# Kernel optimization log

Hardware: AMD Instinct MI355X
Metric: run time of the kernel (lower is better)

Reference implementation:

```python
import jax, jax.numpy as jnp
import numpy as np

TOP_K = 2

def setup_inputs() -> dict:
    key = jax.random.key(0)
    k0, k1, k2, k3 = jax.random.split(key, 4)
    B, S, H, I, E = 2, 2048, 1024, 1408, 8
    hidden_states = jax.random.normal(k0, (B, S, H), dtype=jnp.float32)
    router_weight = jax.random.normal(k1, (E, H), dtype=jnp.float32) * 0.02
    gate_up_proj = jax.random.normal(k2, (E, 2 * I, H), dtype=jnp.float32) * 0.02
    down_proj = jax.random.normal(k3, (E, H, I), dtype=jnp.float32) * 0.02
    return {
        "hidden_states": hidden_states,
        "router_weight": router_weight,
        "gate_up_proj": gate_up_proj,
        "down_proj": down_proj,
    }

def reference(hidden_states, router_weight, gate_up_proj, down_proj):
    B, S, H = hidden_states.shape
    E = router_weight.shape[0]
    x = hidden_states.reshape(-1, H)                       # [T, H]
    T = x.shape[0]
    # Router: logits -> float32 softmax -> top-k (matches torch: topk on probs)
    logits = x @ router_weight.T                           # [T, E]
    probs = jax.nn.softmax(logits.astype(jnp.float32), axis=-1)
    topw, topi = jax.lax.top_k(probs, TOP_K)               # [T, K]
    topw = topw.astype(x.dtype)
    # Per-token combine weights over experts (zero for non-selected experts).
    combine = jnp.zeros((T, E), dtype=x.dtype)
    combine = combine.at[jnp.arange(T)[:, None], topi].set(topw)  # [T, E]
    # Dense grouped expert compute (same math as gather-GEMM-scatter loop:
    # tokens not routed to expert e get combine weight 0).
    gu = jnp.einsum('th,eoh->teo', x, gate_up_proj)        # [T, E, 2I]
    g, u = jnp.split(gu, 2, axis=-1)                       # [T, E, I] each
    h = jax.nn.silu(g) * u                                 # [T, E, I]
    y = jnp.einsum('tei,ehi->teh', h, down_proj)           # [T, E, H]
    out = jnp.einsum('teh,te->th', y, combine)             # [T, H]
    return out.reshape(B, S, H)
```

## Files before the change

### kernel.cpp

```cpp
#include <hip/hip_runtime.h>
#include <math.h>

#define NTOK 4096
#define HDIM 1024
#define NEXP 8
#define IDIM 1408
#define TWO_I 2816
#define TM 256
#define TK 64
#define NRB 40
#define ROWCAP (NRB * 256)

#define RT_BLKS 1024
#define CVG_BLKS 2048
#define G1_BLKS 440
#define CVD_BLKS 256

typedef _Float16 f16x8 __attribute__((ext_vector_type(8)));
typedef float f32x4 __attribute__((ext_vector_type(4)));

typedef __attribute__((address_space(1))) const unsigned int gu32;
typedef __attribute__((address_space(3))) unsigned int lu32;
__device__ __forceinline__ void async16(const void* g, void* l) {
  __builtin_amdgcn_global_load_lds((gu32*)g, (lu32*)l, 16, 0, 0);
}

__device__ __forceinline__ void seg_prefix(const int* __restrict__ counts, int* aof) {
  int o = 0; aof[0] = 0;
#pragma unroll
  for (int i = 0; i < 8; i++) { o += (counts[i] + 255) & ~255; aof[i + 1] = o; }
}

__device__ __forceinline__ void cvt8(const float4* __restrict__ s, uint4* __restrict__ d, size_t idx) {
  float4 a = s[idx * 2], b = s[idx * 2 + 1];
  union { _Float16 h[8]; uint4 u; } p;
  p.h[0] = (_Float16)a.x; p.h[1] = (_Float16)a.y; p.h[2] = (_Float16)a.z; p.h[3] = (_Float16)a.w;
  p.h[4] = (_Float16)b.x; p.h[5] = (_Float16)b.y; p.h[6] = (_Float16)b.z; p.h[7] = (_Float16)b.w;
  d[idx] = p.u;
}

#define NG8 (NEXP * TWO_I * HDIM / 8)
#define ND8 (NEXP * HDIM * IDIM / 8)

extern "C" __global__ void moe_rcv(const float* __restrict__ x,
                                   const float* __restrict__ rw,
                                   int* __restrict__ topi,
                                   float* __restrict__ topw,
                                   _Float16* __restrict__ xh,
                                   const float* __restrict__ gup,
                                   _Float16* __restrict__ guph) {
  if (blockIdx.x >= RT_BLKS) {
    size_t idx = (size_t)(blockIdx.x - RT_BLKS) * 256 + threadIdx.x;
    const float4* s = (const float4*)gup; uint4* d = (uint4*)guph;
    for (; idx < NG8; idx += (size_t)CVG_BLKS * 256) cvt8(s, d, idx);
    return;
  }
  int w = threadIdx.x >> 6, lane = threadIdx.x & 63;
  int t = blockIdx.x * 4 + w;
  const float4* xp = (const float4*)(x + (size_t)t * HDIM);
  const float4* rp = (const float4*)rw;
  float acc[NEXP];
#pragma unroll
  for (int e = 0; e < NEXP; e++) acc[e] = 0.f;
#pragma unroll
  for (int i = 0; i < HDIM / 256; i++) {
    float4 xv = xp[i * 64 + lane];
    union { _Float16 h[4]; uint2 u; } pk;
    pk.h[0] = (_Float16)xv.x; pk.h[1] = (_Float16)xv.y;
    pk.h[2] = (_Float16)xv.z; pk.h[3] = (_Float16)xv.w;
    *(uint2*)(xh + (size_t)t * HDIM + i * 256 + lane * 4) = pk.u;
#pragma unroll
    for (int e = 0; e < NEXP; e++) {
      float4 rv = rp[e * 256 + i * 64 + lane];
      acc[e] += xv.x * rv.x + xv.y * rv.y + xv.z * rv.z + xv.w * rv.w;
    }
  }
#pragma unroll
  for (int e = 0; e < NEXP; e++) {
#pragma unroll
    for (int off = 32; off > 0; off >>= 1) acc[e] += __shfl_down(acc[e], off);
  }
  if (lane == 0) {
    float m = acc[0];
    for (int e = 1; e < NEXP; e++) m = fmaxf(m, acc[e]);
    float p[NEXP], s = 0.f;
    for (int e = 0; e < NEXP; e++) { p[e] = __expf(acc[e] - m); s += p[e]; }
    float inv = 1.f / s;
    int i0 = 0; float b0 = p[0];
    for (int e = 1; e < NEXP; e++) if (p[e] > b0) { b0 = p[e]; i0 = e; }
    int i1 = -1; float b1 = -1.f;
    for (int e = 0; e < NEXP; e++) if (e != i0 && p[e] > b1) { b1 = p[e]; i1 = e; }
    topi[t * 2] = i0; topi[t * 2 + 1] = i1;
    topw[t * 2] = b0 * inv; topw[t * 2 + 1] = b1 * inv;
  }
}

extern "C" __global__ void moe_count(const int* __restrict__ topi, int* __restrict__ cnt_part) {
  __shared__ int cnt[NEXP];
  if (threadIdx.x < NEXP) cnt[threadIdx.x] = 0;
  __syncthreads();
  int t = blockIdx.x * 256 + threadIdx.x;
  atomicAdd(&cnt[topi[t * 2]], 1);
  atomicAdd(&cnt[topi[t * 2 + 1]], 1);
  __syncthreads();
  if (threadIdx.x < NEXP) cnt_part[blockIdx.x * NEXP + threadIdx.x] = cnt[threadIdx.x];
}

extern "C" __global__ void moe_scatter(const int* __restrict__ topi, const float* __restrict__ topw,
                                       const int* __restrict__ cnt_part, int* __restrict__ counts,
                                       int* __restrict__ tok, float* __restrict__ wrow,
                                       int* __restrict__ rows) {
  __shared__ int part_l[16 * NEXP];
  __shared__ int cnt[NEXP];
  __shared__ int base[NEXP];
  __shared__ int tot_l[NEXP];
  const int tid = threadIdx.x, blk = blockIdx.x;
  if (tid < 16 * NEXP) part_l[tid] = cnt_part[tid];
  if (tid < NEXP) cnt[tid] = 0;
  __syncthreads();
  if (tid < NEXP) {
    int tot = 0, pre = 0;
#pragma unroll
    for (int b = 0; b < 16; b++) {
      int v = part_l[b * NEXP + tid];
      tot += v;
      if (b < blk) pre += v;
    }
    tot_l[tid] = tot;
    base[tid] = pre;
  }
  __syncthreads();
  if (tid < NEXP) {
    int o = 0;
    for (int i = 0; i < tid; i++) o += (tot_l[i] + 255) & ~255;
    base[tid] += o;
    if (blk == 0) counts[tid] = tot_l[tid];
  }
  __syncthreads();
  int t = blk * 256 + tid;
  int e0 = topi[t * 2], e1 = topi[t * 2 + 1];
  int r0 = atomicAdd(&cnt[e0], 1);
  int r1 = atomicAdd(&cnt[e1], 1);
  int row0 = base[e0] + r0;
  int row1 = base[e1] + r1;
  tok[row0] = t; wrow[row0] = topw[t * 2];     rows[t * 2]     = row0;
  tok[row1] = t; wrow[row1] = topw[t * 2 + 1]; rows[t * 2 + 1] = row1;
}

#define WAITVM(n) asm volatile("s_waitcnt vmcnt(" #n ")" ::: "memory")
#define BAR() __builtin_amdgcn_s_barrier()
#define PRIO(x) __builtin_amdgcn_s_setprio(x)

#define LDV(off) (*(const f16x8*)((const char*)smem + (uint32_t)(off)))

#define RD_A(grp, BO) { \
  _Pragma("unroll") for (int m_ = 0; m_ < 4; m_++) { \
    va[m_][0] = LDV(sA0 + (BO) + ((grp)*4 + m_)*2048); \
    va[m_][1] = LDV(sA1 + (BO) + ((grp)*4 + m_)*2048); } }

#define RD_B(VB, nb, BO) { \
  _Pragma("unroll") for (int n_ = 0; n_ < 2; n_++) { \
    VB[n_][0] = LDV(sB0 + (BO) + ((nb)*2 + n_)*2048); \
    VB[n_][1] = LDV(sB1 + (BO) + ((nb)*2 + n_)*2048); } }

#define MM(qa, qb, VB) { \
  _Pragma("unroll") for (int k_ = 0; k_ < 2; k_++) \
  _Pragma("unroll") for (int m_ = 0; m_ < 4; m_++) \
  _Pragma("unroll") for (int n_ = 0; n_ < 2; n_++) \
    acc[(qa)*4 + m_][(qb)*2 + n_] = __builtin_amdgcn_mfma_f32_16x16x32_f16( \
        va[m_][k_], VB[n_][k_], acc[(qa)*4 + m_][(qb)*2 + n_], 0, 0, 0); }

#define STG4(P, bf, r0, kt) { \
  async16(P[0][0] + (kt)*TK, smem + ((bf)*4 + (r0))*8192 + wv*512); \
  async16(P[0][1] + (kt)*TK, smem + ((bf)*4 + (r0))*8192 + 4096 + wv*512); \
  async16(P[1][0] + (kt)*TK, smem + ((bf)*4 + (r0) + 1)*8192 + wv*512); \
  async16(P[1][1] + (kt)*TK, smem + ((bf)*4 + (r0) + 1)*8192 + 4096 + wv*512); }
#define STAGE_A(bf, kt) STG4(pA, bf, 0, kt)
#define STAGE_B(bf, kt) STG4(pB, bf, 2, kt)

#define GEMM_CORE(NIT) { \
  STAGE_B(0, 0); STAGE_A(0, 0); \
  STAGE_B(1, 1); STAGE_A(1, 1); \
  WAITVM(8); BAR(); \
  _Pragma("unroll 1") \
  for (int it = 0; it < (NIT); ++it) { \
    const int nl = (it + 1 < (NIT)); \
    const int kt2 = 2*it + 2, kt3 = 2*it + 3; \
     RD_B(vb0, 0, 0); RD_A(0, 0); BAR(); PRIO(1); MM(0,0,vb0); PRIO(0); BAR(); \
     RD_B(vb1, 1, 0); BAR(); PRIO(1); MM(0,1,vb1); PRIO(0); BAR(); \
     RD_A(1, 0); if (nl) STAGE_B(0, kt2); BAR(); PRIO(1); MM(1,0,vb0); PRIO(0); BAR(); \
     if (nl) { STAGE_A(0, kt2); } PRIO(1); MM(1,1,vb1); PRIO(0); \
              if (nl) { WAITVM(8); } else { WAITVM(0); } BAR(); \
     RD_B(vb0, 0, 65536); RD_A(0, 65536); BAR(); PRIO(1); MM(0,0,vb0); PRIO(0); BAR(); \
     RD_B(vb1, 1, 65536); BAR(); PRIO(1); MM(0,1,vb1); PRIO(0); BAR(); \
     RD_A(1, 65536); if (nl) STAGE_B(1, kt3); BAR(); PRIO(1); MM(1,0,vb0); PRIO(0); BAR(); \
     if (nl) { STAGE_A(1, kt3); } PRIO(1); MM(1,1,vb1); PRIO(0); \
              if (nl) { WAITVM(8); } BAR(); \
  } \
  asm volatile("" ::: "memory"); }

#define GEMM_SETUP() \
  const int lane = tid & 63, wv = tid >> 6; \
  const int wm = wv >> 2, wn = wv & 3; \
  const int quad = lane >> 4, l15 = lane & 15; \
  const int srow = tid >> 3; \
  const int kc = ((tid & 7) ^ (srow & 7)) << 3; \
  const uint32_t c0 = (uint32_t)((quad * 16) ^ ((l15 & 7) << 4)); \
  const uint32_t c1 = c0 ^ 64; \
  const uint32_t sA0 = wm * 16384 + l15 * 128 + c0; \
  const uint32_t sA1 = wm * 16384 + l15 * 128 + c1; \
  const uint32_t sB0 = (2 + (wn >> 1)) * 16384 + ((wn & 1) * 64 + l15) * 128 + c0; \
  const uint32_t sB1 = (2 + (wn >> 1)) * 16384 + ((wn & 1) * 64 + l15) * 128 + c1; \
  f32x4 acc[8][4]; \
  _Pragma("unroll") for (int m = 0; m < 8; m++) \
  _Pragma("unroll") for (int n = 0; n < 4; n++) acc[m][n] = (f32x4){0.f, 0.f, 0.f, 0.f}; \
  f16x8 va[4][2], vb0[2][2], vb1[2][2];

extern "C" __global__ __launch_bounds__(512, 2) void moe_gemm1cd(
    const _Float16* __restrict__ xh, const _Float16* __restrict__ guph,
    const int* __restrict__ counts, const int* __restrict__ tok,
    _Float16* __restrict__ hbuf,
    const float* __restrict__ dp, _Float16* __restrict__ dph) {
  __shared__ __align__(128) _Float16 smem[65536];
  const int tid = threadIdx.x;
  const int fid = blockIdx.x;
  if (fid >= G1_BLKS) {
    size_t idx = (size_t)(fid - G1_BLKS) * 512 + tid;
    const float4* s = (const float4*)dp; uint4* d = (uint4*)dph;
    for (; idx < ND8; idx += (size_t)CVD_BLKS * 512) cvt8(s, d, idx);
    return;
  }
  int aof[9]; seg_prefix(counts, aof);
  const int g = fid & 7, t7 = fid >> 3;
  const int j = t7 / 5, r5 = t7 - j * 5;
  const int rb = g + 8 * r5;
  const int row0 = rb * TM;
  if (row0 >= aof[8]) return;
  int e = 0;
#pragma unroll
  for (int i = 0; i < 8; i++) if (row0 >= aof[i]) e = i;
  const int lim = aof[e] + counts[e];

  GEMM_SETUP();

  const _Float16* pA[2][2]; const _Float16* pB[2][2];
#pragma unroll
  for (int h = 0; h < 2; h++)
#pragma unroll
    for (int q = 0; q < 2; q++) {
      int rowi = row0 + h * 128 + q * 64 + srow;
      int tv = tok[rowi];
      int tk = (rowi < lim) ? tv : 0;
      pA[h][q] = xh + (size_t)tk * HDIM + kc;
    }
  const _Float16* eb = guph + (size_t)e * TWO_I * HDIM;
#pragma unroll
  for (int q = 0; q < 2; q++) {
    pB[0][q] = eb + (size_t)(j * 128 + q * 64 + srow) * HDIM + kc;
    pB[1][q] = eb + (size_t)(IDIM + j * 128 + q * 64 + srow) * HDIM + kc;
  }

  GEMM_CORE(HDIM / (2 * TK))

  if (wn >= 2) {
#pragma unroll
    for (int mf = 0; mf < 8; mf++)
#pragma unroll
      for (int nf = 0; nf < 4; nf++)
#pragma unroll
        for (int r2 = 0; r2 < 4; r2++)
          smem[(wm * 128 + mf * 16 + quad * 4 + r2) * 132 + (wn - 2) * 64 + nf * 16 + l15] =
              (_Float16)acc[mf][nf][r2];
  }
  __syncthreads();
  if (wn < 2) {
#pragma unroll
    for (int mf = 0; mf < 8; mf++) {
#pragma unroll
      for (int r2 = 0; r2 < 4; r2++) {
        const int rl = wm * 128 + mf * 16 + quad * 4 + r2;
        _Float16* orow = hbuf + (size_t)(row0 + rl) * IDIM + j * 128 + wn * 64;
#pragma unroll
        for (int nf = 0; nf < 4; nf++) {
          float gg = acc[mf][nf][r2];
          float uu = (float)smem[rl * 132 + wn * 64 + nf * 16 + l15];
          float hh = gg / (1.f + __expf(-gg)) * uu;
          orow[nf * 16 + l15] = (_Float16)hh;
        }
      }
    }
  }
}

extern "C" __global__ __launch_bounds__(256, 2) void moe_gemm2(
    const _Float16* __restrict__ hbuf, const _Float16* __restrict__ dph,
    const int* __restrict__ counts, const float* __restrict__ wrow,
    _Float16* __restrict__ yh) {
  __shared__ __align__(128) _Float16 smem[32768];
  int aof[9]; seg_prefix(counts, aof);
  const int fid = blockIdx.x;
  const int g = fid & 7, t7 = fid >> 3;
  const int cb = t7 / 10, r10 = t7 - cb * 10;
  const int rb = g + 8 * r10;
  const int row0 = rb * 128;
  if (row0 >= aof[8]) return;
  int e = 0;
#pragma unroll
  for (int i = 0; i < 8; i++) if (row0 >= aof[i]) e = i;

  const int tid = threadIdx.x;
  const int lane = tid & 63, wv = tid >> 6;
  const int wm = wv >> 1, wn = wv & 1;
  const int quad = lane >> 4, l15 = lane & 15;
  const int kc = ((tid & 7) ^ ((tid >> 3) & 7)) << 3;
  const uint32_t c0 = (uint32_t)((quad * 16) ^ ((l15 & 7) << 4));
  const uint32_t c1 = c0 ^ 64;
  const uint32_t sA_0 = (uint32_t)((wm * 64 + l15) * 128) + c0;
  const uint32_t sA_1 = (uint32_t)((wm * 64 + l15) * 128) + c1;
  const uint32_t sB_0 = 16384u + (uint32_t)((wn * 64 + l15) * 128) + c0;
  const uint32_t sB_1 = 16384u + (uint32_t)((wn * 64 + l15) * 128) + c1;

  f32x4 acc2[4][4];
#pragma unroll
  for (int m = 0; m < 4; m++)
#pragma unroll
    for (int n = 0; n < 4; n++) acc2[m][n] = (f32x4){0.f, 0.f, 0.f, 0.f};
  f16x8 va2[4][2], vb2[4][2];

  const _Float16* pA2[4]; const _Float16* pB2[4];
  const _Float16* eb = dph + (size_t)e * HDIM * IDIM;
#pragma unroll
  for (int c = 0; c < 4; c++) {
    pA2[c] = hbuf + (size_t)(row0 + c * 32 + (tid >> 3)) * IDIM + kc;
    pB2[c] = eb + (size_t)(cb * 128 + c * 32 + (tid >> 3)) * IDIM + kc;
  }

#define STG2(bf, kt) { \
  _Pragma("unroll") for (int c_ = 0; c_ < 4; c_++) { \
    async16(pA2[c_] + (kt)*TK, smem + (bf)*16384 + c_*2048 + tid*8); \
    async16(pB2[c_] + (kt)*TK, smem + (bf)*16384 + 8192 + c_*2048 + tid*8); } }

  const int NIT2 = IDIM / TK;
  STG2(0, 0); STG2(1, 1);
  WAITVM(8); BAR();
#pragma unroll 1
  for (int kt = 0; kt < NIT2; ++kt) {
    const uint32_t BO = (kt & 1) ? 32768u : 0u;
#pragma unroll
    for (int m_ = 0; m_ < 4; m_++) {
      va2[m_][0] = LDV(sA_0 + BO + m_ * 2048);
      va2[m_][1] = LDV(sA_1 + BO + m_ * 2048);
    }
#pragma unroll
    for (int n_ = 0; n_ < 4; n_++) {
      vb2[n_][0] = LDV(sB_0 + BO + n_ * 2048);
      vb2[n_][1] = LDV(sB_1 + BO + n_ * 2048);
    }
    asm volatile("s_waitcnt lgkmcnt(0)" ::: "memory");
    BAR();
    if (kt + 2 < NIT2) { STG2((kt & 1), kt + 2); }
    PRIO(1);
#pragma unroll
    for (int k_ = 0; k_ < 2; k_++)
#pragma unroll
      for (int m_ = 0; m_ < 4; m_++)
#pragma unroll
        for (int n_ = 0; n_ < 4; n_++)
          acc2[m_][n_] = __builtin_amdgcn_mfma_f32_16x16x32_f16(
              va2[m_][k_], vb2[n_][k_], acc2[m_][n_], 0, 0, 0);
    PRIO(0);
    if (kt + 2 < NIT2) { WAITVM(8); } else { WAITVM(0); }
    BAR();
  }
#undef STG2

#pragma unroll
  for (int mf = 0; mf < 4; mf++) {
#pragma unroll
    for (int r2 = 0; r2 < 4; r2++) {
      const int row = row0 + wm * 64 + mf * 16 + quad * 4 + r2;
      const float wgt = wrow[row];
      _Float16* orow = yh + (size_t)row * HDIM + cb * 128 + wn * 64;
#pragma unroll
      for (int nf = 0; nf < 4; nf++)
        orow[nf * 16 + l15] = (_Float16)(acc2[mf][nf][r2] * wgt);
    }
  }
}

extern "C" __global__ void moe_combine(const _Float16* __restrict__ yh,
                                       const int* __restrict__ rows,
                                       float* __restrict__ out) {
  int i = blockIdx.x * 256 + threadIdx.x;
  int t = i >> 7, c8 = i & 127;
  int rA = rows[t * 2], rB = rows[t * 2 + 1];
  union { uint4 u; _Float16 h[8]; } pa, pb;
  pa.u = ((const uint4*)(yh + (size_t)rA * HDIM))[c8];
  pb.u = ((const uint4*)(yh + (size_t)rB * HDIM))[c8];
  float4 o0, o1;
  o0.x = (float)pa.h[0] + (float)pb.h[0]; o0.y = (float)pa.h[1] + (float)pb.h[1];
  o0.z = (float)pa.h[2] + (float)pb.h[2]; o0.w = (float)pa.h[3] + (float)pb.h[3];
  o1.x = (float)pa.h[4] + (float)pb.h[4]; o1.y = (float)pa.h[5] + (float)pb.h[5];
  o1.z = (float)pa.h[6] + (float)pb.h[6]; o1.w = (float)pa.h[7] + (float)pb.h[7];
  ((float4*)out)[(size_t)i * 2] = o0;
  ((float4*)out)[(size_t)i * 2 + 1] = o1;
}

extern "C" void kernel_launch(void* const* d_in, const int* in_sizes, int n_in,
                              void* d_out, int out_size, void* d_ws, size_t ws_size,
                              hipStream_t stream) {
  const float* x   = (const float*)d_in[0];
  const float* rw  = (const float*)d_in[1];
  const float* gup = (const float*)d_in[2];
  const float* dp  = (const float*)d_in[3];
  float* out = (float*)d_out;

  char* ws = (char*)d_ws;
  int*   counts   = (int*)ws;
  int*   cnt_part = (int*)(ws + 64);
  int*   topi   = (int*)(ws + 4096);
  float* topw   = (float*)(ws + 36864);
  int*   tok    = (int*)(ws + 69632);
  float* wrow   = (float*)(ws + 110592);
  int*   rows   = (int*)(ws + 151552);
  _Float16* xh   = (_Float16*)(ws + 184320);
  _Float16* guph = (_Float16*)(ws + 8572928);
  _Float16* dph  = (_Float16*)(ws + 54710272);
  _Float16* hbuf = (_Float16*)(ws + 77778944);
  _Float16* yh   = (_Float16*)(ws + 8572928);

  moe_rcv<<<RT_BLKS + CVG_BLKS, 256, 0, stream>>>(x, rw, topi, topw, xh, gup, guph);
  moe_count<<<NTOK / 256, 256, 0, stream>>>(topi, cnt_part);
  moe_scatter<<<NTOK / 256, 256, 0, stream>>>(topi, topw, cnt_part, counts, tok, wrow, rows);
  moe_gemm1cd<<<G1_BLKS + CVD_BLKS, 512, 0, stream>>>(xh, guph, counts, tok, hbuf, dp, dph);
  moe_gemm2<<<8 * 8 * 10, 256, 0, stream>>>(hbuf, dph, counts, wrow, yh);
  moe_combine<<<NTOK * HDIM / 8 / 256, 256, 0, stream>>>(yh, rows, out);
}
```

Baseline: 317.1 us.

## Shrink gate-up GEMM tiles to 128x128 and fuse expert counting into router

The first grouped GEMM moves from 256-row tiles with 512-thread blocks and a split-phase schedule to 128-row by 64-column (gate+up) tiles with 256-thread blocks, reusing the simpler double-buffered K-loop shared with the down GEMM. That produces many more blocks (1760 vs 440) and should improve load balance across CUs, but each block reuses less data and runs a simpler pipeline. Expert counting also moves into the router kernel through per-block shared atomics, which removes the separate count launch. The scatter kernel now reduces 1024 partial counts.

```diff
diff --git a/kernel.cpp b/kernel.cpp
--- a/kernel.cpp
+++ b/kernel.cpp
@@ -6,14 +6,13 @@
 #define NEXP 8
 #define IDIM 1408
 #define TWO_I 2816
-#define TM 256
 #define TK 64
-#define NRB 40
-#define ROWCAP (NRB * 256)
+#define ROWCAP 10240
 
 #define RT_BLKS 1024
 #define CVG_BLKS 2048
-#define G1_BLKS 440
+#define G1J 22
+#define G1_BLKS (8 * G1J * 10)
 #define CVD_BLKS 256
 
 typedef _Float16 f16x8 __attribute__((ext_vector_type(8)));
@@ -47,6 +46,7 @@
                                    int* __restrict__ topi,
                                    float* __restrict__ topw,
                                    _Float16* __restrict__ xh,
+                                   int* __restrict__ cnt_part,
                                    const float* __restrict__ gup,
                                    _Float16* __restrict__ guph) {
   if (blockIdx.x >= RT_BLKS) {
@@ -55,6 +55,9 @@
     for (; idx < NG8; idx += (size_t)CVG_BLKS * 256) cvt8(s, d, idx);
     return;
   }
+  __shared__ int c8[NEXP];
+  if (threadIdx.x < NEXP) c8[threadIdx.x] = 0;
+  __syncthreads();
   int w = threadIdx.x >> 6, lane = threadIdx.x & 63;
   int t = blockIdx.x * 4 + w;
   const float4* xp = (const float4*)(x + (size_t)t * HDIM);
@@ -92,37 +95,37 @@
     for (int e = 0; e < NEXP; e++) if (e != i0 && p[e] > b1) { b1 = p[e]; i1 = e; }
     topi[t * 2] = i0; topi[t * 2 + 1] = i1;
     topw[t * 2] = b0 * inv; topw[t * 2 + 1] = b1 * inv;
-  }
-}
-
-extern "C" __global__ void moe_count(const int* __restrict__ topi, int* __restrict__ cnt_part) {
-  __shared__ int cnt[NEXP];
-  if (threadIdx.x < NEXP) cnt[threadIdx.x] = 0;
-  __syncthreads();
-  int t = blockIdx.x * 256 + threadIdx.x;
-  atomicAdd(&cnt[topi[t * 2]], 1);
-  atomicAdd(&cnt[topi[t * 2 + 1]], 1);
-  __syncthreads();
-  if (threadIdx.x < NEXP) cnt_part[blockIdx.x * NEXP + threadIdx.x] = cnt[threadIdx.x];
+    atomicAdd(&c8[i0], 1);
+    atomicAdd(&c8[i1], 1);
+  }
+  __syncthreads();
+  if (threadIdx.x < NEXP) cnt_part[threadIdx.x * 1024 + blockIdx.x] = c8[threadIdx.x];
 }
 
 extern "C" __global__ void moe_scatter(const int* __restrict__ topi, const float* __restrict__ topw,
                                        const int* __restrict__ cnt_part, int* __restrict__ counts,
                                        int* __restrict__ tok, float* __restrict__ wrow,
                                        int* __restrict__ rows) {
-  __shared__ int part_l[16 * NEXP];
+  __shared__ int part16[16 * NEXP];
   __shared__ int cnt[NEXP];
   __shared__ int base[NEXP];
   __shared__ int tot_l[NEXP];
   const int tid = threadIdx.x, blk = blockIdx.x;
-  if (tid < 16 * NEXP) part_l[tid] = cnt_part[tid];
+  if (tid < 128) {
+    int g = tid >> 3, e = tid & 7;
+    const int4* p = (const int4*)(cnt_part + e * 1024 + g * 64);
+    int s = 0;
+#pragma unroll
+    for (int b = 0; b < 16; b++) { int4 v = p[b]; s += v.x + v.y + v.z + v.w; }
+    part16[g * NEXP + e] = s;
+  }
   if (tid < NEXP) cnt[tid] = 0;
   __syncthreads();
   if (tid < NEXP) {
     int tot = 0, pre = 0;
 #pragma unroll
     for (int b = 0; b < 16; b++) {
-      int v = part_l[b * NEXP + tid];
+      int v = part16[b * NEXP + tid];
       tot += v;
       if (b < blk) pre += v;
     }
@@ -150,140 +153,123 @@
 #define WAITVM(n) asm volatile("s_waitcnt vmcnt(" #n ")" ::: "memory")
 #define BAR() __builtin_amdgcn_s_barrier()
 #define PRIO(x) __builtin_amdgcn_s_setprio(x)
-
 #define LDV(off) (*(const f16x8*)((const char*)smem + (uint32_t)(off)))
 
-#define RD_A(grp, BO) { \
-  _Pragma("unroll") for (int m_ = 0; m_ < 4; m_++) { \
-    va[m_][0] = LDV(sA0 + (BO) + ((grp)*4 + m_)*2048); \
-    va[m_][1] = LDV(sA1 + (BO) + ((grp)*4 + m_)*2048); } }
-
-#define RD_B(VB, nb, BO) { \
-  _Pragma("unroll") for (int n_ = 0; n_ < 2; n_++) { \
-    VB[n_][0] = LDV(sB0 + (BO) + ((nb)*2 + n_)*2048); \
-    VB[n_][1] = LDV(sB1 + (BO) + ((nb)*2 + n_)*2048); } }
-
-#define MM(qa, qb, VB) { \
-  _Pragma("unroll") for (int k_ = 0; k_ < 2; k_++) \
-  _Pragma("unroll") for (int m_ = 0; m_ < 4; m_++) \
-  _Pragma("unroll") for (int n_ = 0; n_ < 2; n_++) \
-    acc[(qa)*4 + m_][(qb)*2 + n_] = __builtin_amdgcn_mfma_f32_16x16x32_f16( \
-        va[m_][k_], VB[n_][k_], acc[(qa)*4 + m_][(qb)*2 + n_], 0, 0, 0); }
-
-#define STG4(P, bf, r0, kt) { \
-  async16(P[0][0] + (kt)*TK, smem + ((bf)*4 + (r0))*8192 + wv*512); \
-  async16(P[0][1] + (kt)*TK, smem + ((bf)*4 + (r0))*8192 + 4096 + wv*512); \
-  async16(P[1][0] + (kt)*TK, smem + ((bf)*4 + (r0) + 1)*8192 + wv*512); \
-  async16(P[1][1] + (kt)*TK, smem + ((bf)*4 + (r0) + 1)*8192 + 4096 + wv*512); }
-#define STAGE_A(bf, kt) STG4(pA, bf, 0, kt)
-#define STAGE_B(bf, kt) STG4(pB, bf, 2, kt)
-
-#define GEMM_CORE(NIT) { \
-  STAGE_B(0, 0); STAGE_A(0, 0); \
-  STAGE_B(1, 1); STAGE_A(1, 1); \
+#define STG2(bf, kt) { \
+  _Pragma("unroll") for (int c_ = 0; c_ < 4; c_++) { \
+    async16(pA2[c_] + (size_t)(kt) * TK, smem + (bf) * 16384 + c_ * 2048 + tid * 8); \
+    async16(pB2[c_] + (size_t)(kt) * TK, smem + (bf) * 16384 + 8192 + c_ * 2048 + tid * 8); } }
+
+#define K128_SETUP() \
+  const int lane = tid & 63, wv = tid >> 6; \
+  const int wm = wv >> 1, wn = wv & 1; \
+  const int quad = lane >> 4, l15 = lane & 15; \
+  const int srow8 = tid >> 3; \
+  const int kc = ((tid & 7) ^ (srow8 & 7)) << 3; \
+  const uint32_t c0 = (uint32_t)((quad * 16) ^ ((l15 & 7) << 4)); \
+  const uint32_t c1 = c0 ^ 64; \
+  const uint32_t sA_0 = (uint32_t)((wm * 64 + l15) * 128) + c0; \
+  const uint32_t sA_1 = (uint32_t)((wm * 64 + l15) * 128) + c1; \
+  const uint32_t sB_0 = 16384u + (uint32_t)((wn * 64 + l15) * 128) + c0; \
+  const uint32_t sB_1 = 16384u + (uint32_t)((wn * 64 + l15) * 128) + c1; \
+  f32x4 acc2[4][4]; \
+  _Pragma("unroll") for (int m = 0; m < 4; m++) \
+  _Pragma("unroll") for (int n = 0; n < 4; n++) acc2[m][n] = (f32x4){0.f, 0.f, 0.f, 0.f}; \
+  f16x8 va2[4][2], vb2[4][2];
+
+#define K128_LOOP(NIT) { \
+  STG2(0, 0); STG2(1, 1); \
   WAITVM(8); BAR(); \
   _Pragma("unroll 1") \
-  for (int it = 0; it < (NIT); ++it) { \
-    const int nl = (it + 1 < (NIT)); \
-    const int kt2 = 2*it + 2, kt3 = 2*it + 3; \
-     RD_B(vb0, 0, 0); RD_A(0, 0); BAR(); PRIO(1); MM(0,0,vb0); PRIO(0); BAR(); \
-     RD_B(vb1, 1, 0); BAR(); PRIO(1); MM(0,1,vb1); PRIO(0); BAR(); \
-     RD_A(1, 0); if (nl) STAGE_B(0, kt2); BAR(); PRIO(1); MM(1,0,vb0); PRIO(0); BAR(); \
-     if (nl) { STAGE_A(0, kt2); } PRIO(1); MM(1,1,vb1); PRIO(0); \
-              if (nl) { WAITVM(8); } else { WAITVM(0); } BAR(); \
-     RD_B(vb0, 0, 65536); RD_A(0, 65536); BAR(); PRIO(1); MM(0,0,vb0); PRIO(0); BAR(); \
-     RD_B(vb1, 1, 65536); BAR(); PRIO(1); MM(0,1,vb1); PRIO(0); BAR(); \
-     RD_A(1, 65536); if (nl) STAGE_B(1, kt3); BAR(); PRIO(1); MM(1,0,vb0); PRIO(0); BAR(); \
-     if (nl) { STAGE_A(1, kt3); } PRIO(1); MM(1,1,vb1); PRIO(0); \
-              if (nl) { WAITVM(8); } BAR(); \
-  } \
-  asm volatile("" ::: "memory"); }
-
-#define GEMM_SETUP() \
-  const int lane = tid & 63, wv = tid >> 6; \
-  const int wm = wv >> 2, wn = wv & 3; \
-  const int quad = lane >> 4, l15 = lane & 15; \
-  const int srow = tid >> 3; \
-  const int kc = ((tid & 7) ^ (srow & 7)) << 3; \
-  const uint32_t c0 = (uint32_t)((quad * 16) ^ ((l15 & 7) << 4)); \
-  const uint32_t c1 = c0 ^ 64; \
-  const uint32_t sA0 = wm * 16384 + l15 * 128 + c0; \
-  const uint32_t sA1 = wm * 16384 + l15 * 128 + c1; \
-  const uint32_t sB0 = (2 + (wn >> 1)) * 16384 + ((wn & 1) * 64 + l15) * 128 + c0; \
-  const uint32_t sB1 = (2 + (wn >> 1)) * 16384 + ((wn & 1) * 64 + l15) * 128 + c1; \
-  f32x4 acc[8][4]; \
-  _Pragma("unroll") for (int m = 0; m < 8; m++) \
-  _Pragma("unroll") for (int n = 0; n < 4; n++) acc[m][n] = (f32x4){0.f, 0.f, 0.f, 0.f}; \
-  f16x8 va[4][2], vb0[2][2], vb1[2][2];
-
-extern "C" __global__ __launch_bounds__(512, 2) void moe_gemm1cd(
+  for (int kt = 0; kt < (NIT); ++kt) { \
+    const uint32_t BO = (kt & 1) ? 32768u : 0u; \
+    _Pragma("unroll") for (int m_ = 0; m_ < 4; m_++) { \
+      va2[m_][0] = LDV(sA_0 + BO + m_ * 2048); \
+      va2[m_][1] = LDV(sA_1 + BO + m_ * 2048); } \
+    _Pragma("unroll") for (int n_ = 0; n_ < 4; n_++) { \
+      vb2[n_][0] = LDV(sB_0 + BO + n_ * 2048); \
+      vb2[n_][1] = LDV(sB_1 + BO + n_ * 2048); } \
+    asm volatile("s_waitcnt lgkmcnt(0)" ::: "memory"); \
+    BAR(); \
+    if (kt + 2 < (NIT)) { STG2((kt & 1), kt + 2); } \
+    PRIO(1); \
+    _Pragma("unroll") for (int k_ = 0; k_ < 2; k_++) \
+    _Pragma("unroll") for (int m_ = 0; m_ < 4; m_++) \
+    _Pragma("unroll") for (int n_ = 0; n_ < 4; n_++) \
+      acc2[m_][n_] = __builtin_amdgcn_mfma_f32_16x16x32_f16( \
+          va2[m_][k_], vb2[n_][k_], acc2[m_][n_], 0, 0, 0); \
+    PRIO(0); \
+    if (kt + 2 < (NIT)) { WAITVM(8); } else { WAITVM(0); } \
+    BAR(); \
+  } }
+
+extern "C" __global__ __launch_bounds__(256, 2) void moe_gemm1cd(
     const _Float16* __restrict__ xh, const _Float16* __restrict__ guph,
     const int* __restrict__ counts, const int* __restrict__ tok,
     _Float16* __restrict__ hbuf,
     const float* __restrict__ dp, _Float16* __restrict__ dph) {
-  __shared__ __align__(128) _Float16 smem[65536];
+  __shared__ __align__(128) _Float16 smem[32768];
   const int tid = threadIdx.x;
   const int fid = blockIdx.x;
   if (fid >= G1_BLKS) {
-    size_t idx = (size_t)(fid - G1_BLKS) * 512 + tid;
+    size_t idx = (size_t)(fid - G1_BLKS) * 256 + tid;
     const float4* s = (const float4*)dp; uint4* d = (uint4*)dph;
-    for (; idx < ND8; idx += (size_t)CVD_BLKS * 512) cvt8(s, d, idx);
+    for (; idx < ND8; idx += (size_t)CVD_BLKS * 256) cvt8(s, d, idx);
     return;
   }
   int aof[9]; seg_prefix(counts, aof);
   const int g = fid & 7, t7 = fid >> 3;
-  const int j = t7 / 5, r5 = t7 - j * 5;
-  const int rb = g + 8 * r5;
-  const int row0 = rb * TM;
+  const int j = t7 / 10, r10 = t7 - j * 10;
+  const int rb = g + 8 * r10;
+  const int row0 = rb * 128;
   if (row0 >= aof[8]) return;
   int e = 0;
 #pragma unroll
   for (int i = 0; i < 8; i++) if (row0 >= aof[i]) e = i;
   const int lim = aof[e] + counts[e];
 
-  GEMM_SETUP();
-
-  const _Float16* pA[2][2]; const _Float16* pB[2][2];
-#pragma unroll
-  for (int h = 0; h < 2; h++)
-#pragma unroll
-    for (int q = 0; q < 2; q++) {
-      int rowi = row0 + h * 128 + q * 64 + srow;
-      int tv = tok[rowi];
-      int tk = (rowi < lim) ? tv : 0;
-      pA[h][q] = xh + (size_t)tk * HDIM + kc;
-    }
+  K128_SETUP();
+
+  const _Float16* pA2[4]; const _Float16* pB2[4];
+#pragma unroll
+  for (int c = 0; c < 4; c++) {
+    int rowi = row0 + c * 32 + srow8;
+    int tv = tok[rowi];
+    int tk = (rowi < lim) ? tv : 0;
+    pA2[c] = xh + (size_t)tk * HDIM + kc;
+  }
   const _Float16* eb = guph + (size_t)e * TWO_I * HDIM;
 #pragma unroll
-  for (int q = 0; q < 2; q++) {
-    pB[0][q] = eb + (size_t)(j * 128 + q * 64 + srow) * HDIM + kc;
-    pB[1][q] = eb + (size_t)(IDIM + j * 128 + q * 64 + srow) * HDIM + kc;
-  }
-
-  GEMM_CORE(HDIM / (2 * TK))
-
-  if (wn >= 2) {
-#pragma unroll
-    for (int mf = 0; mf < 8; mf++)
+  for (int c = 0; c < 4; c++) {
+    int brow = (c < 2) ? (j * 64 + c * 32 + srow8)
+                       : (IDIM + j * 64 + (c - 2) * 32 + srow8);
+    pB2[c] = eb + (size_t)brow * HDIM + kc;
+  }
+
+  K128_LOOP(HDIM / TK)
+
+  if (wn == 1) {
+#pragma unroll
+    for (int mf = 0; mf < 4; mf++)
 #pragma unroll
       for (int nf = 0; nf < 4; nf++)
 #pragma unroll
         for (int r2 = 0; r2 < 4; r2++)
-          smem[(wm * 128 + mf * 16 + quad * 4 + r2) * 132 + (wn - 2) * 64 + nf * 16 + l15] =
-              (_Float16)acc[mf][nf][r2];
-  }
-  __syncthreads();
-  if (wn < 2) {
-#pragma unroll
-    for (int mf = 0; mf < 8; mf++) {
+          smem[(wm * 64 + mf * 16 + quad * 4 + r2) * 66 + nf * 16 + l15] =
+              (_Float16)acc2[mf][nf][r2];
+  }
+  __syncthreads();
+  if (wn == 0) {
+#pragma unroll
+    for (int mf = 0; mf < 4; mf++) {
 #pragma unroll
       for (int r2 = 0; r2 < 4; r2++) {
-        const int rl = wm * 128 + mf * 16 + quad * 4 + r2;
-        _Float16* orow = hbuf + (size_t)(row0 + rl) * IDIM + j * 128 + wn * 64;
+        const int rl = wm * 64 + mf * 16 + quad * 4 + r2;
+        _Float16* orow = hbuf + (size_t)(row0 + rl) * IDIM + j * 64;
 #pragma unroll
         for (int nf = 0; nf < 4; nf++) {
-          float gg = acc[mf][nf][r2];
-          float uu = (float)smem[rl * 132 + wn * 64 + nf * 16 + l15];
+          float gg = acc2[mf][nf][r2];
+          float uu = (float)smem[rl * 66 + nf * 16 + l15];
           float hh = gg / (1.f + __expf(-gg)) * uu;
           orow[nf * 16 + l15] = (_Float16)hh;
         }
@@ -309,70 +295,17 @@
   for (int i = 0; i < 8; i++) if (row0 >= aof[i]) e = i;
 
   const int tid = threadIdx.x;
-  const int lane = tid & 63, wv = tid >> 6;
-  const int wm = wv >> 1, wn = wv & 1;
-  const int quad = lane >> 4, l15 = lane & 15;
-  const int kc = ((tid & 7) ^ ((tid >> 3) & 7)) << 3;
-  const uint32_t c0 = (uint32_t)((quad * 16) ^ ((l15 & 7) << 4));
-  const uint32_t c1 = c0 ^ 64;
-  const uint32_t sA_0 = (uint32_t)((wm * 64 + l15) * 128) + c0;
-  const uint32_t sA_1 = (uint32_t)((wm * 64 + l15) * 128) + c1;
-  const uint32_t sB_0 = 16384u + (uint32_t)((wn * 64 + l15) * 128) + c0;
-  const uint32_t sB_1 = 16384u + (uint32_t)((wn * 64 + l15) * 128) + c1;
-
-  f32x4 acc2[4][4];
-#pragma unroll
-  for (int m = 0; m < 4; m++)
-#pragma unroll
-    for (int n = 0; n < 4; n++) acc2[m][n] = (f32x4){0.f, 0.f, 0.f, 0.f};
-  f16x8 va2[4][2], vb2[4][2];
+  K128_SETUP();
 
   const _Float16* pA2[4]; const _Float16* pB2[4];
   const _Float16* eb = dph + (size_t)e * HDIM * IDIM;
 #pragma unroll
   for (int c = 0; c < 4; c++) {
-    pA2[c] = hbuf + (size_t)(row0 + c * 32 + (tid >> 3)) * IDIM + kc;
-    pB2[c] = eb + (size_t)(cb * 128 + c * 32 + (tid >> 3)) * IDIM + kc;
-  }
-
-#define STG2(bf, kt) { \
-  _Pragma("unroll") for (int c_ = 0; c_ < 4; c_++) { \
-    async16(pA2[c_] + (kt)*TK, smem + (bf)*16384 + c_*2048 + tid*8); \
-    async16(pB2[c_] + (kt)*TK, smem + (bf)*16384 + 8192 + c_*2048 + tid*8); } }
-
-  const int NIT2 = IDIM / TK;
-  STG2(0, 0); STG2(1, 1);
-  WAITVM(8); BAR();
-#pragma unroll 1
-  for (int kt = 0; kt < NIT2; ++kt) {
-    const uint32_t BO = (kt & 1) ? 32768u : 0u;
-#pragma unroll
-    for (int m_ = 0; m_ < 4; m_++) {
-      va2[m_][0] = LDV(sA_0 + BO + m_ * 2048);
-      va2[m_][1] = LDV(sA_1 + BO + m_ * 2048);
-    }
-#pragma unroll
-    for (int n_ = 0; n_ < 4; n_++) {
-      vb2[n_][0] = LDV(sB_0 + BO + n_ * 2048);
-      vb2[n_][1] = LDV(sB_1 + BO + n_ * 2048);
-    }
-    asm volatile("s_waitcnt lgkmcnt(0)" ::: "memory");
-    BAR();
-    if (kt + 2 < NIT2) { STG2((kt & 1), kt + 2); }
-    PRIO(1);
-#pragma unroll
-    for (int k_ = 0; k_ < 2; k_++)
-#pragma unroll
-      for (int m_ = 0; m_ < 4; m_++)
-#pragma unroll
-        for (int n_ = 0; n_ < 4; n_++)
-          acc2[m_][n_] = __builtin_amdgcn_mfma_f32_16x16x32_f16(
-              va2[m_][k_], vb2[n_][k_], acc2[m_][n_], 0, 0, 0);
-    PRIO(0);
-    if (kt + 2 < NIT2) { WAITVM(8); } else { WAITVM(0); }
-    BAR();
-  }
-#undef STG2
+    pA2[c] = hbuf + (size_t)(row0 + c * 32 + srow8) * IDIM + kc;
+    pB2[c] = eb + (size_t)(cb * 128 + c * 32 + srow8) * IDIM + kc;
+  }
+
+  K128_LOOP(IDIM / TK)
 
 #pragma unroll
   for (int mf = 0; mf < 4; mf++) {
@@ -418,21 +351,20 @@
   char* ws = (char*)d_ws;
   int*   counts   = (int*)ws;
   int*   cnt_part = (int*)(ws + 64);
-  int*   topi   = (int*)(ws + 4096);
-  float* topw   = (float*)(ws + 36864);
-  int*   tok    = (int*)(ws + 69632);
-  float* wrow   = (float*)(ws + 110592);
-  int*   rows   = (int*)(ws + 151552);
-  _Float16* xh   = (_Float16*)(ws + 184320);
-  _Float16* guph = (_Float16*)(ws + 8572928);
-  _Float16* dph  = (_Float16*)(ws + 54710272);
-  _Float16* hbuf = (_Float16*)(ws + 77778944);
-  _Float16* yh   = (_Float16*)(ws + 8572928);
-
-  moe_rcv<<<RT_BLKS + CVG_BLKS, 256, 0, stream>>>(x, rw, topi, topw, xh, gup, guph);
-  moe_count<<<NTOK / 256, 256, 0, stream>>>(topi, cnt_part);
+  int*   topi   = (int*)(ws + 32832);
+  float* topw   = (float*)(ws + 65600);
+  int*   tok    = (int*)(ws + 98368);
+  float* wrow   = (float*)(ws + 139328);
+  int*   rows   = (int*)(ws + 180288);
+  _Float16* xh   = (_Float16*)(ws + 213056);
+  _Float16* guph = (_Float16*)(ws + 8601664);
+  _Float16* dph  = (_Float16*)(ws + 54739008);
+  _Float16* hbuf = (_Float16*)(ws + 77807680);
+  _Float16* yh   = (_Float16*)(ws + 8601664);
+
+  moe_rcv<<<RT_BLKS + CVG_BLKS, 256, 0, stream>>>(x, rw, topi, topw, xh, cnt_part, gup, guph);
   moe_scatter<<<NTOK / 256, 256, 0, stream>>>(topi, topw, cnt_part, counts, tok, wrow, rows);
-  moe_gemm1cd<<<G1_BLKS + CVD_BLKS, 512, 0, stream>>>(xh, guph, counts, tok, hbuf, dp, dph);
+  moe_gemm1cd<<<G1_BLKS + CVD_BLKS, 256, 0, stream>>>(xh, guph, counts, tok, hbuf, dp, dph);
   moe_gemm2<<<8 * 8 * 10, 256, 0, stream>>>(hbuf, dph, counts, wrow, yh);
   moe_combine<<<NTOK * HDIM / 8 / 256, 256, 0, stream>>>(yh, rows, out);
 }
```

New measurement: 347.6 us. 1.1x slower.

## Fuse expert counting into router, retile down-projection GEMM to 256x256 tiles

Applied to the files above, without the earlier changes.

Expert counting moves into the router kernel: each router block writes per-block counts, and the scatter kernel reduces them, so the separate count launch goes away. The down-projection GEMM changes from 128x128 tiles with 256 threads to the shared 256x256, 512-thread GEMM core used by the first GEMM, which raises data reuse per block but leaves fewer blocks to fill the device. The row-block to block-index mapping also changes from interleaved to contiguous, which may affect L2 locality.

```diff
diff --git a/kernel.cpp b/kernel.cpp
--- a/kernel.cpp
+++ b/kernel.cpp
@@ -47,6 +47,7 @@
                                    int* __restrict__ topi,
                                    float* __restrict__ topw,
                                    _Float16* __restrict__ xh,
+                                   int* __restrict__ cnt_part,
                                    const float* __restrict__ gup,
                                    _Float16* __restrict__ guph) {
   if (blockIdx.x >= RT_BLKS) {
@@ -55,6 +56,9 @@
     for (; idx < NG8; idx += (size_t)CVG_BLKS * 256) cvt8(s, d, idx);
     return;
   }
+  __shared__ int c8[NEXP];
+  if (threadIdx.x < NEXP) c8[threadIdx.x] = 0;
+  __syncthreads();
   int w = threadIdx.x >> 6, lane = threadIdx.x & 63;
   int t = blockIdx.x * 4 + w;
   const float4* xp = (const float4*)(x + (size_t)t * HDIM);
@@ -92,37 +96,37 @@
     for (int e = 0; e < NEXP; e++) if (e != i0 && p[e] > b1) { b1 = p[e]; i1 = e; }
     topi[t * 2] = i0; topi[t * 2 + 1] = i1;
     topw[t * 2] = b0 * inv; topw[t * 2 + 1] = b1 * inv;
-  }
-}
-
-extern "C" __global__ void moe_count(const int* __restrict__ topi, int* __restrict__ cnt_part) {
-  __shared__ int cnt[NEXP];
-  if (threadIdx.x < NEXP) cnt[threadIdx.x] = 0;
-  __syncthreads();
-  int t = blockIdx.x * 256 + threadIdx.x;
-  atomicAdd(&cnt[topi[t * 2]], 1);
-  atomicAdd(&cnt[topi[t * 2 + 1]], 1);
-  __syncthreads();
-  if (threadIdx.x < NEXP) cnt_part[blockIdx.x * NEXP + threadIdx.x] = cnt[threadIdx.x];
+    atomicAdd(&c8[i0], 1);
+    atomicAdd(&c8[i1], 1);
+  }
+  __syncthreads();
+  if (threadIdx.x < NEXP) cnt_part[threadIdx.x * 1024 + blockIdx.x] = c8[threadIdx.x];
 }
 
 extern "C" __global__ void moe_scatter(const int* __restrict__ topi, const float* __restrict__ topw,
                                        const int* __restrict__ cnt_part, int* __restrict__ counts,
                                        int* __restrict__ tok, float* __restrict__ wrow,
                                        int* __restrict__ rows) {
-  __shared__ int part_l[16 * NEXP];
+  __shared__ int part16[16 * NEXP];
   __shared__ int cnt[NEXP];
   __shared__ int base[NEXP];
   __shared__ int tot_l[NEXP];
   const int tid = threadIdx.x, blk = blockIdx.x;
-  if (tid < 16 * NEXP) part_l[tid] = cnt_part[tid];
+  if (tid < 128) {
+    int g = tid >> 3, e = tid & 7;
+    const int4* p = (const int4*)(cnt_part + e * 1024 + g * 64);
+    int s = 0;
+#pragma unroll
+    for (int b = 0; b < 16; b++) { int4 v = p[b]; s += v.x + v.y + v.z + v.w; }
+    part16[g * NEXP + e] = s;
+  }
   if (tid < NEXP) cnt[tid] = 0;
   __syncthreads();
   if (tid < NEXP) {
     int tot = 0, pre = 0;
 #pragma unroll
     for (int b = 0; b < 16; b++) {
-      int v = part_l[b * NEXP + tid];
+      int v = part16[b * NEXP + tid];
       tot += v;
       if (b < blk) pre += v;
     }
@@ -231,9 +235,9 @@
     return;
   }
   int aof[9]; seg_prefix(counts, aof);
-  const int g = fid & 7, t7 = fid >> 3;
-  const int j = t7 / 5, r5 = t7 - j * 5;
-  const int rb = g + 8 * r5;
+  const int g = fid & 7, idx = fid >> 3;
+  const int j = idx / 5, r = idx - j * 5;
+  const int rb = g * 5 + r;
   const int row0 = rb * TM;
   if (row0 >= aof[8]) return;
   int e = 0;
@@ -292,98 +296,50 @@
   }
 }
 
-extern "C" __global__ __launch_bounds__(256, 2) void moe_gemm2(
+extern "C" __global__ __launch_bounds__(512, 2) void moe_gemm2(
     const _Float16* __restrict__ hbuf, const _Float16* __restrict__ dph,
     const int* __restrict__ counts, const float* __restrict__ wrow,
     _Float16* __restrict__ yh) {
-  __shared__ __align__(128) _Float16 smem[32768];
+  __shared__ __align__(128) _Float16 smem[65536];
   int aof[9]; seg_prefix(counts, aof);
+  const int tid = threadIdx.x;
   const int fid = blockIdx.x;
-  const int g = fid & 7, t7 = fid >> 3;
-  const int cb = t7 / 10, r10 = t7 - cb * 10;
-  const int rb = g + 8 * r10;
-  const int row0 = rb * 128;
+  const int g = fid & 7, idx = fid >> 3;
+  const int cb = idx / 5, r = idx - cb * 5;
+  const int rb = g * 5 + r;
+  const int row0 = rb * TM;
   if (row0 >= aof[8]) return;
   int e = 0;
 #pragma unroll
   for (int i = 0; i < 8; i++) if (row0 >= aof[i]) e = i;
 
-  const int tid = threadIdx.x;
-  const int lane = tid & 63, wv = tid >> 6;
-  const int wm = wv >> 1, wn = wv & 1;
-  const int quad = lane >> 4, l15 = lane & 15;
-  const int kc = ((tid & 7) ^ ((tid >> 3) & 7)) << 3;
-  const uint32_t c0 = (uint32_t)((quad * 16) ^ ((l15 & 7) << 4));
-  const uint32_t c1 = c0 ^ 64;
-  const uint32_t sA_0 = (uint32_t)((wm * 64 + l15) * 128) + c0;
-  const uint32_t sA_1 = (uint32_t)((wm * 64 + l15) * 128) + c1;
-  const uint32_t sB_0 = 16384u + (uint32_t)((wn * 64 + l15) * 128) + c0;
-  const uint32_t sB_1 = 16384u + (uint32_t)((wn * 64 + l15) * 128) + c1;
-
-  f32x4 acc2[4][4];
-#pragma unroll
-  for (int m = 0; m < 4; m++)
-#pragma unroll
-    for (int n = 0; n < 4; n++) acc2[m][n] = (f32x4){0.f, 0.f, 0.f, 0.f};
-  f16x8 va2[4][2], vb2[4][2];
-
-  const _Float16* pA2[4]; const _Float16* pB2[4];
+  GEMM_SETUP();
+
+  const _Float16* pA[2][2]; const _Float16* pB[2][2];
+#pragma unroll
+  for (int h = 0; h < 2; h++)
+#pragma unroll
+    for (int q = 0; q < 2; q++)
+      pA[h][q] = hbuf + (size_t)(row0 + h * 128 + q * 64 + srow) * IDIM + kc;
   const _Float16* eb = dph + (size_t)e * HDIM * IDIM;
 #pragma unroll
-  for (int c = 0; c < 4; c++) {
-    pA2[c] = hbuf + (size_t)(row0 + c * 32 + (tid >> 3)) * IDIM + kc;
-    pB2[c] = eb + (size_t)(cb * 128 + c * 32 + (tid >> 3)) * IDIM + kc;
-  }
-
-#define STG2(bf, kt) { \
-  _Pragma("unroll") for (int c_ = 0; c_ < 4; c_++) { \
-    async16(pA2[c_] + (kt)*TK, smem + (bf)*16384 + c_*2048 + tid*8); \
-    async16(pB2[c_] + (kt)*TK, smem + (bf)*16384 + 8192 + c_*2048 + tid*8); } }
-
-  const int NIT2 = IDIM / TK;
-  STG2(0, 0); STG2(1, 1);
-  WAITVM(8); BAR();
-#pragma unroll 1
-  for (int kt = 0; kt < NIT2; ++kt) {
-    const uint32_t BO = (kt & 1) ? 32768u : 0u;
-#pragma unroll
-    for (int m_ = 0; m_ < 4; m_++) {
-      va2[m_][0] = LDV(sA_0 + BO + m_ * 2048);
-      va2[m_][1] = LDV(sA_1 + BO + m_ * 2048);
-    }
-#pragma unroll
-    for (int n_ = 0; n_ < 4; n_++) {
-      vb2[n_][0] = LDV(sB_0 + BO + n_ * 2048);
-      vb2[n_][1] = LDV(sB_1 + BO + n_ * 2048);
-    }
-    asm volatile("s_waitcnt lgkmcnt(0)" ::: "memory");
-    BAR();
-    if (kt + 2 < NIT2) { STG2((kt & 1), kt + 2); }
-    PRIO(1);
-#pragma unroll
-    for (int k_ = 0; k_ < 2; k_++)
-#pragma unroll
-      for (int m_ = 0; m_ < 4; m_++)
-#pragma unroll
-        for (int n_ = 0; n_ < 4; n_++)
-          acc2[m_][n_] = __builtin_amdgcn_mfma_f32_16x16x32_f16(
-              va2[m_][k_], vb2[n_][k_], acc2[m_][n_], 0, 0, 0);
-    PRIO(0);
-    if (kt + 2 < NIT2) { WAITVM(8); } else { WAITVM(0); }
-    BAR();
-  }
-#undef STG2
-
-#pragma unroll
-  for (int mf = 0; mf < 4; mf++) {
+  for (int h = 0; h < 2; h++)
+#pragma unroll
+    for (int q = 0; q < 2; q++)
+      pB[h][q] = eb + (size_t)(cb * 256 + h * 128 + q * 64 + srow) * IDIM + kc;
+
+  GEMM_CORE(IDIM / (2 * TK))
+
+#pragma unroll
+  for (int mf = 0; mf < 8; mf++) {
 #pragma unroll
     for (int r2 = 0; r2 < 4; r2++) {
-      const int row = row0 + wm * 64 + mf * 16 + quad * 4 + r2;
+      const int row = row0 + wm * 128 + mf * 16 + quad * 4 + r2;
       const float wgt = wrow[row];
-      _Float16* orow = yh + (size_t)row * HDIM + cb * 128 + wn * 64;
+      _Float16* orow = yh + (size_t)row * HDIM + cb * 256 + wn * 64;
 #pragma unroll
       for (int nf = 0; nf < 4; nf++)
-        orow[nf * 16 + l15] = (_Float16)(acc2[mf][nf][r2] * wgt);
+        orow[nf * 16 + l15] = (_Float16)(acc[mf][nf][r2] * wgt);
     }
   }
 }
@@ -418,21 +374,20 @@
   char* ws = (char*)d_ws;
   int*   counts   = (int*)ws;
   int*   cnt_part = (int*)(ws + 64);
-  int*   topi   = (int*)(ws + 4096);
-  float* topw   = (float*)(ws + 36864);
-  int*   tok    = (int*)(ws + 69632);
-  float* wrow   = (float*)(ws + 110592);
-  int*   rows   = (int*)(ws + 151552);
-  _Float16* xh   = (_Float16*)(ws + 184320);
-  _Float16* guph = (_Float16*)(ws + 8572928);
-  _Float16* dph  = (_Float16*)(ws + 54710272);
-  _Float16* hbuf = (_Float16*)(ws + 77778944);
-  _Float16* yh   = (_Float16*)(ws + 8572928);
-
-  moe_rcv<<<RT_BLKS + CVG_BLKS, 256, 0, stream>>>(x, rw, topi, topw, xh, gup, guph);
-  moe_count<<<NTOK / 256, 256, 0, stream>>>(topi, cnt_part);
+  int*   topi   = (int*)(ws + 32832);
+  float* topw   = (float*)(ws + 65600);
+  int*   tok    = (int*)(ws + 98368);
+  float* wrow   = (float*)(ws + 139328);
+  int*   rows   = (int*)(ws + 180288);
+  _Float16* xh   = (_Float16*)(ws + 213056);
+  _Float16* guph = (_Float16*)(ws + 8601664);
+  _Float16* dph  = (_Float16*)(ws + 54739008);
+  _Float16* hbuf = (_Float16*)(ws + 77807680);
+  _Float16* yh   = (_Float16*)(ws + 8601664);
+
+  moe_rcv<<<RT_BLKS + CVG_BLKS, 256, 0, stream>>>(x, rw, topi, topw, xh, cnt_part, gup, guph);
   moe_scatter<<<NTOK / 256, 256, 0, stream>>>(topi, topw, cnt_part, counts, tok, wrow, rows);
   moe_gemm1cd<<<G1_BLKS + CVD_BLKS, 512, 0, stream>>>(xh, guph, counts, tok, hbuf, dp, dph);
-  moe_gemm2<<<8 * 8 * 10, 256, 0, stream>>>(hbuf, dph, counts, wrow, yh);
+  moe_gemm2<<<8 * 4 * 5, 512, 0, stream>>>(hbuf, dph, counts, wrow, yh);
   moe_combine<<<NTOK * HDIM / 8 / 256, 256, 0, stream>>>(yh, rows, out);
 }
```

Result: no change. 322.0 us (+1.5%).
